# Performance work log

Measured on AMD Instinct MI355X. Metric: run time of the kernel, lower is better.

The kernel has to match this reference:

```python
import jax, jax.numpy as jnp
import numpy as np

B, S, D, H = 2, 2048, 2048, 16
HD = D // H  # head_dim = 128


def setup_inputs() -> dict:
    key = jax.random.key(0)
    ks = jax.random.split(key, 9)
    std = 0.02
    x = jax.random.normal(ks[0], (B, S, D), dtype=jnp.float32)
    Wq = jax.random.normal(ks[1], (D, D), dtype=jnp.float32) * std
    bq = jnp.zeros((D,), dtype=jnp.float32)
    Wk = jax.random.normal(ks[2], (D, D), dtype=jnp.float32) * std
    bk = jnp.zeros((D,), dtype=jnp.float32)
    Wv = jax.random.normal(ks[3], (D, D), dtype=jnp.float32) * std
    bv = jnp.zeros((D,), dtype=jnp.float32)
    Wo = jax.random.normal(ks[4], (D, D), dtype=jnp.float32) * std
    bo = jnp.zeros((D,), dtype=jnp.float32)
    return {"x": x, "Wq": Wq, "bq": bq, "Wk": Wk, "bk": bk,
            "Wv": Wv, "bv": bv, "Wo": Wo, "bo": bo}


def _rope_tables(seq_len, head_dim, base=10000.0):
    # inv_freq over even indices; freqs: [S, HD/2]
    inv_freq = 1.0 / (base ** (jnp.arange(0, head_dim, 2, dtype=jnp.float32) / head_dim))
    t = jnp.arange(seq_len, dtype=jnp.float32)
    freqs = jnp.einsum('i,j->ij', t, inv_freq)
    return jnp.cos(freqs), jnp.sin(freqs)  # each [S, HD/2]


def _rotate(x, cos, sin):
    # x: [B, H, S, HD]; cos/sin: [S, HD/2] broadcast over B,H
    x1, x2 = jnp.split(x, 2, axis=-1)
    return jnp.concatenate([x1 * cos - x2 * sin, x1 * sin + x2 * cos], axis=-1)


def reference(x, Wq, bq, Wk, bk, Wv, bv, Wo, bo):
    b, s, d = x.shape
    q = (jnp.einsum('bsd,df->bsf', x, Wq) + bq).reshape(b, s, H, HD).transpose(0, 2, 1, 3)
    k = (jnp.einsum('bsd,df->bsf', x, Wk) + bk).reshape(b, s, H, HD).transpose(0, 2, 1, 3)
    v = (jnp.einsum('bsd,df->bsf', x, Wv) + bv).reshape(b, s, H, HD).transpose(0, 2, 1, 3)
    cos, sin = _rope_tables(s, HD)
    qr = _rotate(q, cos, sin)
    kr = _rotate(k, cos, sin)
    scores = jnp.einsum('bhqd,bhkd->bhqk', qr, kr) / jnp.sqrt(jnp.float32(HD))
    probs = jax.nn.softmax(scores, axis=-1)
    out = jnp.einsum('bhqk,bhkd->bhqd', probs, v)
    out = out.transpose(0, 2, 1, 3).reshape(b, s, d)
    return jnp.einsum('bsd,df->bsf', out, Wo) + bo
```

## Files before the change

### kernel.cpp

```cpp
#include <hip/hip_runtime.h>

#define BB  2
#define SS  2048
#define DD  2048
#define HH  16
#define HDD 128
#define BSR 4096

using short8  = __attribute__((ext_vector_type(8))) short;
using floatx4 = __attribute__((ext_vector_type(4))) float;

__device__ __forceinline__ float bf2f(unsigned short u) {
  return __uint_as_float(((unsigned int)u) << 16);
}
__device__ __forceinline__ unsigned short f2bf(float f) {
  unsigned int u = __float_as_uint(f);
  u += 0x7fffu + ((u >> 16) & 1u);
  return (unsigned short)(u >> 16);
}
__device__ __forceinline__ unsigned int pk2bf(float a, float b) {
  unsigned int ua = __float_as_uint(a);
  ua += 0x7fffu + ((ua >> 16) & 1u);
  unsigned int ub = __float_as_uint(b);
  ub += 0x7fffu + ((ub >> 16) & 1u);
  return (ua >> 16) | (ub & 0xffff0000u);
}
__device__ __forceinline__ float fexp2(float x) {
#if __has_builtin(__builtin_amdgcn_exp2f)
  return __builtin_amdgcn_exp2f(x);
#else
  return __expf(x * 0.6931471805599453f);
#endif
}
__device__ __forceinline__ void gl_lds16(const void* g, void* l) {
  __builtin_amdgcn_global_load_lds(
      (__attribute__((address_space(1))) void*)g,
      (__attribute__((address_space(3))) void*)l, 16, 0, 0);
}

__global__ __launch_bounds__(256) void prep(
    const float* __restrict__ x,
    const float* __restrict__ Wq, const float* __restrict__ Wk,
    const float* __restrict__ Wv, const float* __restrict__ Wo,
    unsigned short* __restrict__ xb,
    unsigned short* __restrict__ wqkvt, unsigned short* __restrict__ wot,
    float2* __restrict__ rtab)
{
  __shared__ float tile[32][33];
  int bid = blockIdx.x;
  int t = threadIdx.x;
  if (bid < 16384) {
    int z = bid >> 12;
    int rem = bid & 4095;
    int by = rem >> 6, bx = rem & 63;
    const float* W; unsigned short* Out;
    if      (z == 0) { W = Wq; Out = wqkvt; }
    else if (z == 1) { W = Wk; Out = wqkvt + (size_t)DD * DD; }
    else if (z == 2) { W = Wv; Out = wqkvt + 2 * (size_t)DD * DD; }
    else             { W = Wo; Out = wot; }
    int tx = t & 31, ty = t >> 5;
    int d0 = by * 32, f0 = bx * 32;
#pragma unroll
    for (int i = 0; i < 4; i++)
      tile[ty + i * 8][tx] = W[(size_t)(d0 + ty + i * 8) * DD + f0 + tx];
    __syncthreads();
#pragma unroll
    for (int i = 0; i < 4; i++)
      Out[(size_t)(f0 + ty + i * 8) * DD + d0 + tx] = f2bf(tile[tx][ty + i * 8]);
  } else if (bid < 16384 + 8192) {
    size_t i = ((size_t)(bid - 16384) * 256 + t) * 4;
    float4 v = *(const float4*)(x + i);
    ushort4 o;
    o.x = f2bf(v.x); o.y = f2bf(v.y); o.z = f2bf(v.z); o.w = f2bf(v.w);
    *(ushort4*)(xb + i) = o;
  } else {
    int idx = (bid - 24576) * 256 + t;
    int s = idx >> 6, c = idx & 63;
    float inv = powf(10000.f, -(float)c * (1.f / 64.f));
    float ang = (float)s * inv;
    float sn, cc;
    sincosf(ang, &sn, &cc);
    rtab[idx] = make_float2(cc, sn);
  }
}

__global__ __launch_bounds__(256) void gemm_qkv(
    const unsigned short* __restrict__ A, const unsigned short* __restrict__ Bt,
    const float* __restrict__ bq, const float* __restrict__ bk,
    const float* __restrict__ bv, const float2* __restrict__ rtab,
    unsigned short* __restrict__ q_r, unsigned short* __restrict__ k_r,
    unsigned short* __restrict__ v_t)
{
  __shared__ unsigned short smem[16896];
  unsigned short* As = smem;
  unsigned short* Bs = smem + 8192;
  const int K = DD;
  int t = threadIdx.x;
  int m0 = blockIdx.y * 128, n0 = blockIdx.x * 128;
  int w = t >> 6, lane = t & 63, qd = lane >> 4, l16 = lane & 15;
  int wm = (w >> 1) * 64, wn = (w & 1) * 64;
  floatx4 zero4 = {0.f, 0.f, 0.f, 0.f};
  floatx4 acc[4][4];
#pragma unroll
  for (int i = 0; i < 4; i++)
#pragma unroll
    for (int j = 0; j < 4; j++) acc[i][j] = zero4;

  int gchunk = (t & 7) ^ ((t >> 3) & 7);
  const unsigned short* Ab = A  + (size_t)(m0 + (t >> 3)) * K + gchunk * 8;
  const unsigned short* Bb = Bt + (size_t)(n0 + (t >> 3)) * K + gchunk * 8;
  size_t qK = (size_t)32 * K;

  for (int k0 = 0; k0 < K; k0 += 64) {
    __syncthreads();
#pragma unroll
    for (int c = 0; c < 4; c++) {
      gl_lds16(Ab + c * qK + k0, &As[(c * 256 + t) * 8]);
      gl_lds16(Bb + c * qK + k0, &Bs[(c * 256 + t) * 8]);
    }
    __syncthreads();
#pragma unroll
    for (int ks = 0; ks < 2; ks++) {
      int ch = ((ks * 4 + qd) ^ (l16 & 7)) * 8;
      short8 af[4], bfr[4];
#pragma unroll
      for (int i = 0; i < 4; i++)
        af[i] = *(const short8*)&As[(wm + i * 16 + l16) * 64 + ch];
#pragma unroll
      for (int j = 0; j < 4; j++)
        bfr[j] = *(const short8*)&Bs[(wn + j * 16 + l16) * 64 + ch];
#pragma unroll
      for (int i = 0; i < 4; i++)
#pragma unroll
        for (int j = 0; j < 4; j++)
          acc[i][j] = __builtin_amdgcn_mfma_f32_16x16x32_bf16(af[i], bfr[j], acc[i][j], 0, 0, 0);
    }
  }

  int plane = n0 >> 11;
  int h = (n0 >> 7) & 15;
  const float* bias = plane == 0 ? bq : (plane == 1 ? bk : bv);
  __syncthreads();
#pragma unroll
  for (int i = 0; i < 4; i++)
#pragma unroll
    for (int j = 0; j < 4; j++) {
      int rl = wm + i * 16 + qd * 4;
      int cl = wn + j * 16 + l16;
      float bsv = bias[h * 128 + cl];
#pragma unroll
      for (int r = 0; r < 4; r++)
        smem[(rl + r) * 132 + cl] = f2bf(acc[i][j][r] + bsv);
    }
  __syncthreads();

  int b = m0 >> 11, sbase = m0 & (SS - 1);
  if (plane < 2) {
    unsigned short* dst = (plane == 0 ? q_r : k_r) + (size_t)(b * HH + h) * SS * HDD;
    const float fac = (plane == 0) ? 0.12751744f : 1.0f;
#pragma unroll
    for (int it = 0; it < 16; it++) {
      int idx = it * 256 + t;
      int rl = idx >> 5, c2 = (idx & 31) * 2;
      int s = sbase + rl;
      float4 cs = *(const float4*)&rtab[(size_t)s * 64 + c2];
      float a0 = bf2f(smem[rl * 132 + c2]);
      float a1 = bf2f(smem[rl * 132 + c2 + 1]);
      float b0 = bf2f(smem[rl * 132 + c2 + 64]);
      float b1 = bf2f(smem[rl * 132 + c2 + 65]);
      unsigned int lo = pk2bf((a0 * cs.x - b0 * cs.y) * fac,
                              (a1 * cs.z - b1 * cs.w) * fac);
      unsigned int hi = pk2bf((a0 * cs.y + b0 * cs.x) * fac,
                              (a1 * cs.w + b1 * cs.z) * fac);
      size_t rowb = (size_t)s * HDD;
      *(unsigned int*)&dst[rowb + c2]      = lo;
      *(unsigned int*)&dst[rowb + c2 + 64] = hi;
    }
  } else {
    unsigned short* dst = v_t + (size_t)(b * HH + h) * HDD * SS;
#pragma unroll
    for (int it = 0; it < 32; it++) {
      int idx = it * 256 + t;
      int hd = idx >> 6, sp = (idx & 63) * 2;
      unsigned short v0 = smem[sp * 132 + hd];
      unsigned short v1 = smem[(sp + 1) * 132 + hd];
      int y = sp & 63;
      int kap = ((y >> 5) & 1) * 32 + ((y >> 2) & 3) * 8 + ((y >> 4) & 1) * 4 + (y & 3);
      int sg = sbase + (sp & ~63) + kap;
      *(unsigned int*)&dst[(size_t)hd * SS + sg] = ((unsigned int)v1 << 16) | v0;
    }
  }
}

template <bool OUTF32>
__global__ __launch_bounds__(256) void gemm_bt(
    const unsigned short* __restrict__ A, const unsigned short* __restrict__ Bt,
    const float* __restrict__ bias, void* __restrict__ Cout,
    int M, int N, int K)
{
  __shared__ unsigned short As[128 * 64];
  __shared__ unsigned short Bs[128 * 64];
  int t = threadIdx.x;
  int m0 = blockIdx.y * 128, n0 = blockIdx.x * 128;
  int w = t >> 6, lane = t & 63, qd = lane >> 4, l16 = lane & 15;
  int wm = (w >> 1) * 64, wn = (w & 1) * 64;
  floatx4 zero4 = {0.f, 0.f, 0.f, 0.f};
  floatx4 acc[4][4];
#pragma unroll
  for (int i = 0; i < 4; i++)
#pragma unroll
    for (int j = 0; j < 4; j++) acc[i][j] = zero4;

  int gchunk = (t & 7) ^ ((t >> 3) & 7);
  const unsigned short* Ab = A  + (size_t)(m0 + (t >> 3)) * K + gchunk * 8;
  const unsigned short* Bb = Bt + (size_t)(n0 + (t >> 3)) * K + gchunk * 8;
  size_t qK = (size_t)32 * K;

  for (int k0 = 0; k0 < K; k0 += 64) {
    __syncthreads();
#pragma unroll
    for (int c = 0; c < 4; c++) {
      gl_lds16(Ab + c * qK + k0, &As[(c * 256 + t) * 8]);
      gl_lds16(Bb + c * qK + k0, &Bs[(c * 256 + t) * 8]);
    }
    __syncthreads();
#pragma unroll
    for (int ks = 0; ks < 2; ks++) {
      int ch = ((ks * 4 + qd) ^ (l16 & 7)) * 8;
      short8 af[4], bfr[4];
#pragma unroll
      for (int i = 0; i < 4; i++)
        af[i] = *(const short8*)&As[(wm + i * 16 + l16) * 64 + ch];
#pragma unroll
      for (int j = 0; j < 4; j++)
        bfr[j] = *(const short8*)&Bs[(wn + j * 16 + l16) * 64 + ch];
#pragma unroll
      for (int i = 0; i < 4; i++)
#pragma unroll
        for (int j = 0; j < 4; j++)
          acc[i][j] = __builtin_amdgcn_mfma_f32_16x16x32_bf16(af[i], bfr[j], acc[i][j], 0, 0, 0);
    }
  }

#pragma unroll
  for (int i = 0; i < 4; i++)
#pragma unroll
    for (int j = 0; j < 4; j++) {
      int row = m0 + wm + i * 16 + qd * 4;
      int col = n0 + wn + j * 16 + l16;
      float bsv = bias ? bias[col] : 0.f;
#pragma unroll
      for (int r = 0; r < 4; r++) {
        float v = acc[i][j][r] + bsv;
        if (OUTF32) ((float*)Cout)[(size_t)(row + r) * N + col] = v;
        else ((unsigned short*)Cout)[(size_t)(row + r) * N + col] = f2bf(v);
      }
    }
}

__global__ __launch_bounds__(256, 2) void attn_kernel(
    const unsigned short* __restrict__ q_r, const unsigned short* __restrict__ k_r,
    const unsigned short* __restrict__ v_t, unsigned short* __restrict__ aout)
{
  __shared__ unsigned short Ks[2][64 * 128];
  __shared__ unsigned short Vs[2][128 * 64];
  int t = threadIdx.x, w = t >> 6, lane = t & 63, qd = lane >> 4, l16 = lane & 15;
  int L = blockIdx.y * gridDim.x + blockIdx.x;
  int jj = L >> 3;
  int bh = (L & 7) * 4 + (jj >> 4);
  int q0 = (jj & 15) * 128;
  const unsigned short* qb = q_r + (size_t)bh * SS * HDD;
  const unsigned short* kb = k_r + (size_t)bh * SS * HDD;
  const unsigned short* vb = v_t + (size_t)bh * HDD * SS;

  short8 aq[2][4];
#pragma unroll
  for (int mi = 0; mi < 2; mi++)
#pragma unroll
    for (int ks = 0; ks < 4; ks++)
      aq[mi][ks] = *(const short8*)
          &qb[(size_t)(q0 + w * 32 + mi * 16 + l16) * HDD + ks * 32 + qd * 8];

  float m_i[2], l_i[2];
  floatx4 zero4 = {0.f, 0.f, 0.f, 0.f};
  floatx4 o[2][8];
#pragma unroll
  for (int mi = 0; mi < 2; mi++) { m_i[mi] = -1e30f; l_i[mi] = 0.f; }
#pragma unroll
  for (int mi = 0; mi < 2; mi++)
#pragma unroll
    for (int n = 0; n < 8; n++) o[mi][n] = zero4;

  auto stage = [&](int nb, int kt) {
#pragma unroll
    for (int c = 0; c < 4; c++) {
      int flat = c * 256 + t;
      int r = flat >> 4, cc = flat & 15;
      gl_lds16(kb + (size_t)(kt + r) * HDD + (cc ^ (r & 15)) * 8, &Ks[nb][flat * 8]);
    }
#pragma unroll
    for (int c = 0; c < 4; c++) {
      int flat = c * 256 + t;
      int r = flat >> 3, cc = flat & 7;
      gl_lds16(vb + (size_t)r * SS + kt + (cc ^ (r & 7)) * 8, &Vs[nb][flat * 8]);
    }
  };

  stage(0, 0);
  int buf = 0;

  for (int kt = 0; kt < SS; kt += 64) {
    __syncthreads();
    if (kt + 64 < SS) stage(buf ^ 1, kt + 64);

    floatx4 sc[2][4];
#pragma unroll
    for (int mi = 0; mi < 2; mi++)
#pragma unroll
      for (int j = 0; j < 4; j++) sc[mi][j] = zero4;
    __builtin_amdgcn_s_setprio(1);
#pragma unroll
    for (int j = 0; j < 4; j++) {
      int krow = j * 16 + l16;
#pragma unroll
      for (int ks = 0; ks < 4; ks++) {
        int chunk = ks * 4 + qd;
        short8 kf = *(const short8*)&Ks[buf][krow * 128 + ((chunk ^ (krow & 15)) * 8)];
        sc[0][j] = __builtin_amdgcn_mfma_f32_16x16x32_bf16(kf, aq[0][ks], sc[0][j], 0, 0, 0);
        sc[1][j] = __builtin_amdgcn_mfma_f32_16x16x32_bf16(kf, aq[1][ks], sc[1][j], 0, 0, 0);
      }
    }
    __builtin_amdgcn_s_setprio(0);

    float rmax[2];
#pragma unroll
    for (int mi = 0; mi < 2; mi++) {
      float m = sc[mi][0][0];
#pragma unroll
      for (int j = 0; j < 4; j++)
#pragma unroll
        for (int r = 0; r < 4; r++) m = fmaxf(m, sc[mi][j][r]);
      m = fmaxf(m, __shfl_xor(m, 16, 64));
      m = fmaxf(m, __shfl_xor(m, 32, 64));
      rmax[mi] = m;
    }

    bool up = (rmax[0] > m_i[0]) || (rmax[1] > m_i[1]);
    if (__ballot(up) != 0ull) {
#pragma unroll
      for (int mi = 0; mi < 2; mi++) {
        float mn = fmaxf(m_i[mi], rmax[mi]);
        float a = fexp2(m_i[mi] - mn);
        m_i[mi] = mn;
        l_i[mi] *= a;
#pragma unroll
        for (int n = 0; n < 8; n++)
#pragma unroll
          for (int r = 0; r < 4; r++) o[mi][n][r] *= a;
      }
    }

    unsigned int pr[2][4][2];
#pragma unroll
    for (int mi = 0; mi < 2; mi++) {
      float s0 = 0.f;
#pragma unroll
      for (int j = 0; j < 4; j++) {
        float p0 = fexp2(sc[mi][j][0] - m_i[mi]);
        float p1 = fexp2(sc[mi][j][1] - m_i[mi]);
        float p2 = fexp2(sc[mi][j][2] - m_i[mi]);
        float p3 = fexp2(sc[mi][j][3] - m_i[mi]);
        s0 += (p0 + p1) + (p2 + p3);
        pr[mi][j][0] = pk2bf(p0, p1);
        pr[mi][j][1] = pk2bf(p2, p3);
      }
      s0 += __shfl_xor(s0, 16, 64);
      s0 += __shfl_xor(s0, 32, 64);
      l_i[mi] += s0;
    }

    __builtin_amdgcn_s_setprio(1);
#pragma unroll
    for (int n = 0; n < 8; n++) {
      int vrow = n * 16 + l16;
#pragma unroll
      for (int ks = 0; ks < 2; ks++) {
        int chunk = ks * 4 + qd;
        short8 av = *(const short8*)&Vs[buf][vrow * 64 + ((chunk ^ (vrow & 7)) * 8)];
        union { unsigned int u[4]; short8 v; } bp0, bp1;
        bp0.u[0] = pr[0][2 * ks][0];     bp0.u[1] = pr[0][2 * ks][1];
        bp0.u[2] = pr[0][2 * ks + 1][0]; bp0.u[3] = pr[0][2 * ks + 1][1];
        bp1.u[0] = pr[1][2 * ks][0];     bp1.u[1] = pr[1][2 * ks][1];
        bp1.u[2] = pr[1][2 * ks + 1][0]; bp1.u[3] = pr[1][2 * ks + 1][1];
        o[0][n] = __builtin_amdgcn_mfma_f32_16x16x32_bf16(av, bp0.v, o[0][n], 0, 0, 0);
        o[1][n] = __builtin_amdgcn_mfma_f32_16x16x32_bf16(av, bp1.v, o[1][n], 0, 0, 0);
      }
    }
    __builtin_amdgcn_s_setprio(0);
    buf ^= 1;
  }

  int b = bh >> 4, h = bh & 15;
#pragma unroll
  for (int mi = 0; mi < 2; mi++) {
    int qrow = q0 + w * 32 + mi * 16 + l16;
    float inv_l = 1.f / l_i[mi];
    size_t base = ((size_t)(b * SS + qrow)) * DD + h * HDD;
#pragma unroll
    for (int n = 0; n < 8; n++) {
      uint2 pkd;
      pkd.x = pk2bf(o[mi][n][0] * inv_l, o[mi][n][1] * inv_l);
      pkd.y = pk2bf(o[mi][n][2] * inv_l, o[mi][n][3] * inv_l);
      *(uint2*)&aout[base + n * 16 + qd * 4] = pkd;
    }
  }
}

extern "C" void kernel_launch(void* const* d_in, const int* in_sizes, int n_in,
                              void* d_out, int out_size, void* d_ws, size_t ws_size,
                              hipStream_t stream) {
  const float* x  = (const float*)d_in[0];
  const float* Wq = (const float*)d_in[1];
  const float* bq = (const float*)d_in[2];
  const float* Wk = (const float*)d_in[3];
  const float* bk = (const float*)d_in[4];
  const float* Wv = (const float*)d_in[5];
  const float* bv = (const float*)d_in[6];
  const float* Wo = (const float*)d_in[7];
  const float* bo = (const float*)d_in[8];
  float* out = (float*)d_out;

  char* ws = (char*)d_ws;
  unsigned short* xb      = (unsigned short*)(ws + 0);
  unsigned short* wqkvt   = (unsigned short*)(ws + 16777216);
  unsigned short* wot     = (unsigned short*)(ws + 41943040);
  float2*         rtab    = (float2*)(ws + 50331648);
  unsigned short* q_r     = (unsigned short*)(ws + 100663296);
  unsigned short* k_r     = (unsigned short*)(ws + 117440512);
  unsigned short* v_t     = (unsigned short*)(ws + 134217728);
  unsigned short* attn_o  = xb;

  prep<<<dim3(25088), dim3(256), 0, stream>>>(
      x, Wq, Wk, Wv, Wo, xb, wqkvt, wot, rtab);
  gemm_qkv<<<dim3(3 * DD / 128, BSR / 128), dim3(256), 0, stream>>>(
      xb, wqkvt, bq, bk, bv, rtab, q_r, k_r, v_t);
  attn_kernel<<<dim3(SS / 128, BB * HH), dim3(256), 0, stream>>>(
      q_r, k_r, v_t, attn_o);
  gemm_bt<true><<<dim3(DD / 128, BSR / 128), dim3(256), 0, stream>>>(
      attn_o, wot, bo, out, BSR, DD, DD);
}
```

Before: 392.3 us.

## Load K/V fragments directly from global and widen weight transpose tiles

```diff
diff --git a/kernel.cpp b/kernel.cpp
--- a/kernel.cpp
+++ b/kernel.cpp
@@ -46,35 +46,44 @@
     unsigned short* __restrict__ wqkvt, unsigned short* __restrict__ wot,
     float2* __restrict__ rtab)
 {
-  __shared__ float tile[32][33];
+  __shared__ float tile[64][65];
   int bid = blockIdx.x;
   int t = threadIdx.x;
-  if (bid < 16384) {
-    int z = bid >> 12;
-    int rem = bid & 4095;
-    int by = rem >> 6, bx = rem & 63;
+  if (bid < 4096) {
+    int z = bid >> 10;
+    int rem = bid & 1023;
+    int by = rem >> 5, bx = rem & 31;
     const float* W; unsigned short* Out;
     if      (z == 0) { W = Wq; Out = wqkvt; }
     else if (z == 1) { W = Wk; Out = wqkvt + (size_t)DD * DD; }
     else if (z == 2) { W = Wv; Out = wqkvt + 2 * (size_t)DD * DD; }
     else             { W = Wo; Out = wot; }
-    int tx = t & 31, ty = t >> 5;
-    int d0 = by * 32, f0 = bx * 32;
-#pragma unroll
-    for (int i = 0; i < 4; i++)
-      tile[ty + i * 8][tx] = W[(size_t)(d0 + ty + i * 8) * DD + f0 + tx];
+    int d0 = by * 64, f0 = bx * 64;
+    int rr = t >> 4, c4 = (t & 15) * 4;
+#pragma unroll
+    for (int i = 0; i < 4; i++) {
+      int row = rr + i * 16;
+      float4 v = *(const float4*)&W[(size_t)(d0 + row) * DD + f0 + c4];
+      tile[row][c4] = v.x; tile[row][c4 + 1] = v.y;
+      tile[row][c4 + 2] = v.z; tile[row][c4 + 3] = v.w;
+    }
     __syncthreads();
 #pragma unroll
-    for (int i = 0; i < 4; i++)
-      Out[(size_t)(f0 + ty + i * 8) * DD + d0 + tx] = f2bf(tile[tx][ty + i * 8]);
-  } else if (bid < 16384 + 8192) {
-    size_t i = ((size_t)(bid - 16384) * 256 + t) * 4;
+    for (int i = 0; i < 4; i++) {
+      int f = rr + i * 16;
+      ushort4 o4;
+      o4.x = f2bf(tile[c4][f]);     o4.y = f2bf(tile[c4 + 1][f]);
+      o4.z = f2bf(tile[c4 + 2][f]); o4.w = f2bf(tile[c4 + 3][f]);
+      *(ushort4*)&Out[(size_t)(f0 + f) * DD + d0 + c4] = o4;
+    }
+  } else if (bid < 4096 + 8192) {
+    size_t i = ((size_t)(bid - 4096) * 256 + t) * 4;
     float4 v = *(const float4*)(x + i);
     ushort4 o;
     o.x = f2bf(v.x); o.y = f2bf(v.y); o.z = f2bf(v.z); o.w = f2bf(v.w);
     *(ushort4*)(xb + i) = o;
   } else {
-    int idx = (bid - 24576) * 256 + t;
+    int idx = (bid - 12288) * 256 + t;
     int s = idx >> 6, c = idx & 63;
     float inv = powf(10000.f, -(float)c * (1.f / 64.f));
     float ang = (float)s * inv;
@@ -262,8 +271,6 @@
     const unsigned short* __restrict__ q_r, const unsigned short* __restrict__ k_r,
     const unsigned short* __restrict__ v_t, unsigned short* __restrict__ aout)
 {
-  __shared__ unsigned short Ks[2][64 * 128];
-  __shared__ unsigned short Vs[2][128 * 64];
   int t = threadIdx.x, w = t >> 6, lane = t & 63, qd = lane >> 4, l16 = lane & 15;
   int L = blockIdx.y * gridDim.x + blockIdx.x;
   int jj = L >> 3;
@@ -291,28 +298,8 @@
 #pragma unroll
     for (int n = 0; n < 8; n++) o[mi][n] = zero4;
 
-  auto stage = [&](int nb, int kt) {
-#pragma unroll
-    for (int c = 0; c < 4; c++) {
-      int flat = c * 256 + t;
-      int r = flat >> 4, cc = flat & 15;
-      gl_lds16(kb + (size_t)(kt + r) * HDD + (cc ^ (r & 15)) * 8, &Ks[nb][flat * 8]);
-    }
-#pragma unroll
-    for (int c = 0; c < 4; c++) {
-      int flat = c * 256 + t;
-      int r = flat >> 3, cc = flat & 7;
-      gl_lds16(vb + (size_t)r * SS + kt + (cc ^ (r & 7)) * 8, &Vs[nb][flat * 8]);
-    }
-  };
-
-  stage(0, 0);
-  int buf = 0;
-
+#pragma unroll 1
   for (int kt = 0; kt < SS; kt += 64) {
-    __syncthreads();
-    if (kt + 64 < SS) stage(buf ^ 1, kt + 64);
-
     floatx4 sc[2][4];
 #pragma unroll
     for (int mi = 0; mi < 2; mi++)
@@ -321,11 +308,10 @@
     __builtin_amdgcn_s_setprio(1);
 #pragma unroll
     for (int j = 0; j < 4; j++) {
-      int krow = j * 16 + l16;
+      const unsigned short* kp = kb + (size_t)(kt + j * 16 + l16) * HDD + qd * 8;
 #pragma unroll
       for (int ks = 0; ks < 4; ks++) {
-        int chunk = ks * 4 + qd;
-        short8 kf = *(const short8*)&Ks[buf][krow * 128 + ((chunk ^ (krow & 15)) * 8)];
+        short8 kf = *(const short8*)(kp + ks * 32);
         sc[0][j] = __builtin_amdgcn_mfma_f32_16x16x32_bf16(kf, aq[0][ks], sc[0][j], 0, 0, 0);
         sc[1][j] = __builtin_amdgcn_mfma_f32_16x16x32_bf16(kf, aq[1][ks], sc[1][j], 0, 0, 0);
       }
@@ -382,11 +368,10 @@
     __builtin_amdgcn_s_setprio(1);
 #pragma unroll
     for (int n = 0; n < 8; n++) {
-      int vrow = n * 16 + l16;
+      const unsigned short* vp = vb + (size_t)(n * 16 + l16) * SS + kt + qd * 8;
 #pragma unroll
       for (int ks = 0; ks < 2; ks++) {
-        int chunk = ks * 4 + qd;
-        short8 av = *(const short8*)&Vs[buf][vrow * 64 + ((chunk ^ (vrow & 7)) * 8)];
+        short8 av = *(const short8*)(vp + ks * 32);
         union { unsigned int u[4]; short8 v; } bp0, bp1;
         bp0.u[0] = pr[0][2 * ks][0];     bp0.u[1] = pr[0][2 * ks][1];
         bp0.u[2] = pr[0][2 * ks + 1][0]; bp0.u[3] = pr[0][2 * ks + 1][1];
@@ -397,7 +382,6 @@
       }
     }
     __builtin_amdgcn_s_setprio(0);
-    buf ^= 1;
   }
 
   int b = bh >> 4, h = bh & 15;
@@ -440,7 +424,7 @@
   unsigned short* v_t     = (unsigned short*)(ws + 134217728);
   unsigned short* attn_o  = xb;
 
-  prep<<<dim3(25088), dim3(256), 0, stream>>>(
+  prep<<<dim3(12800), dim3(256), 0, stream>>>(
       x, Wq, Wk, Wv, Wo, xb, wqkvt, wot, rtab);
   gemm_qkv<<<dim3(3 * DD / 128, BSR / 128), dim3(256), 0, stream>>>(
       xb, wqkvt, bq, bk, bv, rtab, q_r, k_r, v_t);
```

Measured after the change: 540.2 us. 1.38x slower.
